# Optimization experiments

Hardware: AMD Instinct MI355X
Metric: run time of the kernel (lower is better)

Reference implementation:

```python
import jax, jax.numpy as jnp
import numpy as np

B = 131072
D_IN = 128
D_H = 128


def _linear_params(key, fan_in, fan_out):
    # mimic nn.Linear init: U(-1/sqrt(fan_in), 1/sqrt(fan_in))
    kw, kb = jax.random.split(key)
    bound = 1.0 / np.sqrt(fan_in)
    W = jax.random.uniform(kw, (fan_in, fan_out), minval=-bound, maxval=bound, dtype=jnp.float32)
    b = jax.random.uniform(kb, (fan_out,), minval=-bound, maxval=bound, dtype=jnp.float32)
    return W, b


def setup_inputs() -> dict:
    key = jax.random.key(0)
    ks = jax.random.split(key, 12)
    inp = {
        'input': jax.random.normal(ks[0], (B, D_IN), dtype=jnp.float32),
        'seq_input': jax.random.normal(ks[1], (B, D_IN), dtype=jnp.float32),
        'hidden': jax.random.normal(ks[2], (B, D_H), dtype=jnp.float32),
    }
    names = ['ir', 'iz', 'in_', 'sr', 'sz', 'sn', 'hr', 'hz', 'hn']
    for i, nm in enumerate(names):
        fan_in = D_H if nm.startswith('h') else D_IN
        W, b = _linear_params(ks[3 + i], fan_in, D_H)
        inp['W_' + nm] = W
        inp['b_' + nm] = b
    return inp


def reference(input, seq_input, hidden,
              W_ir, b_ir, W_iz, b_iz, W_in_, b_in_,
              W_sr, b_sr, W_sz, b_sz, W_sn, b_sn,
              W_hr, b_hr, W_hz, b_hz, W_hn, b_hn):
    def lin(x, W, b):
        return x @ W + b

    hr = lin(hidden, W_hr, b_hr)  # shared between r_input and r_seq
    r_input = jax.nn.sigmoid(lin(input, W_ir, b_ir) + hr)
    r_seq = jax.nn.sigmoid(lin(seq_input, W_sr, b_sr) + hr)
    r = (r_input + r_seq) * 0.5

    hz = lin(hidden, W_hz, b_hz)
    z_input = jax.nn.sigmoid(lin(input, W_iz, b_iz) + hz)
    z_seq = jax.nn.sigmoid(lin(seq_input, W_sz, b_sz) + hz)
    z = (z_input + z_seq) * 0.5

    n = jnp.tanh(lin(input, W_in_, b_in_) + lin(seq_input, W_sn, b_sn)
                 + lin(r * hidden, W_hn, b_hn))
    new_hidden = (1.0 - z) * n + z * hidden
    return new_hidden
```

## Files before the change

kernel.cpp:

```cpp
#include <hip/hip_runtime.h>

#define BDIM 512
#define PACK_BDIM 256

typedef __attribute__((ext_vector_type(8))) short bf16x8;
typedef __attribute__((ext_vector_type(4))) float f32x4;
typedef __attribute__((ext_vector_type(4))) unsigned int u32x4;

__device__ __forceinline__ unsigned short f2b(float x) {
    unsigned u = __float_as_uint(x);
    return (unsigned short)((u + 0x7fffu + ((u >> 16) & 1u)) >> 16);
}
__device__ __forceinline__ float b2f(unsigned short b) {
    return __uint_as_float(((unsigned)b) << 16);
}

typedef __attribute__((address_space(1))) const unsigned int ga_u32;
typedef __attribute__((address_space(3))) unsigned int la_u32;
__device__ __forceinline__ void gload_lds16(const void* g, void* l) {
    __builtin_amdgcn_global_load_lds((ga_u32*)g, (la_u32*)l, 16, 0, 0);
}

__global__ __launch_bounds__(PACK_BDIM) void pack_weights(
    const float* __restrict__ w0, const float* __restrict__ w1,
    const float* __restrict__ w2, const float* __restrict__ w3,
    const float* __restrict__ w4, const float* __restrict__ w5,
    const float* __restrict__ w6, const float* __restrict__ w7,
    const float* __restrict__ w8,
    const float* __restrict__ b0, const float* __restrict__ b1,
    const float* __restrict__ b2, const float* __restrict__ b3,
    const float* __restrict__ b4, const float* __restrict__ b5,
    const float* __restrict__ b6, const float* __restrict__ b7,
    const float* __restrict__ b8, unsigned short* __restrict__ wp)
{
    __shared__ float wsm[16384];
    const float* W; const float* Bp;
    switch (blockIdx.x) {
        case 0: W = w0; Bp = b0; break; case 1: W = w1; Bp = b1; break;
        case 2: W = w2; Bp = b2; break; case 3: W = w3; Bp = b3; break;
        case 4: W = w4; Bp = b4; break; case 5: W = w5; Bp = b5; break;
        case 6: W = w6; Bp = b6; break; case 7: W = w7; Bp = b7; break;
        default: W = w8; Bp = b8; break;
    }
    const int tid = threadIdx.x;
    for (int i = tid; i < 16384; i += PACK_BDIM) wsm[i] = W[i];
    float* biasf = (float*)(wp + 294912);
    if (tid < 128) biasf[blockIdx.x * 128 + tid] = Bp[tid];
    __syncthreads();
    unsigned short* dst = wp + (size_t)blockIdx.x * 32768;
    for (int item = tid; item < 4096; item += PACK_BDIM) {
        const int lane = item & 63, q = item >> 6;
        const int s = q >> 5, cf = q & 31, c = cf >> 3, f = cf & 7;
        const int k0 = c * 32 + (lane >> 4) * 8;
        const int n  = f * 16 + (lane & 15);
        unsigned v2[4];
        for (int i2 = 0; i2 < 4; i2++) {
            unsigned short lohi[2];
            for (int t = 0; t < 2; t++) {
                float x = wsm[(k0 + i2 * 2 + t) * 128 + n];
                unsigned short hb = f2b(x);
                if (s) { hb = (unsigned short)(__float_as_uint(x - b2f(hb)) >> 16); }
                lohi[t] = hb;
            }
            v2[i2] = (unsigned)lohi[0] | ((unsigned)lohi[1] << 16);
        }
        u32x4 vv; vv[0] = v2[0]; vv[1] = v2[1]; vv[2] = v2[2]; vv[3] = v2[3];
        *(u32x4*)(dst + (size_t)(s * 32 + cf) * 512 + lane * 8) = vv;
    }
}

__global__ __launch_bounds__(BDIM) __attribute__((amdgpu_waves_per_eu(4)))
void gru_fused(
    const float* __restrict__ inp, const float* __restrict__ seqp,
    const float* __restrict__ hid, const unsigned short* __restrict__ wp,
    float* __restrict__ outp)
{
    __shared__ __align__(16) unsigned short wbuf[2][16384];
    float* tb = (float*)wbuf[1];

    const int tid    = threadIdx.x;
    const int lane   = tid & 63;
    const int wid    = tid >> 6;
    const int rowgrp = wid >> 1;
    const int colgrp = wid & 1;
    const int agrp   = lane >> 4;
    const int a16    = lane & 15;
    const int ncol0  = colgrp * 64;
    const size_t row0 = (size_t)blockIdx.x * 64;
    const int locrow_a = rowgrp * 16 + a16;
    const int rswA = (locrow_a & 7) << 3;

    const float* pAin  = inp  + (row0 + locrow_a) * 128;
    const float* pAseq = seqp + (row0 + locrow_a) * 128;
    const float* pAhid = hid  + (row0 + locrow_a) * 128;
    const float* biasf = (const float*)(wp + 294912);

    f32x4 hx[4], s1[4], nacc[4], G[4];
    u32x4 ahs[4];
    const f32x4 zv = {0.f, 0.f, 0.f, 0.f};

    auto stageu = [&](int g, int s, int b) {
        const char* src = (const char*)wp + (size_t)g * 65536 + (size_t)s * 32768;
        char* dstb = (char*)wbuf[b];
        #pragma unroll
        for (int j = 0; j < 4; j++) {
            const int off = (j * 8 + wid) * 1024;
            gload_lds16(src + off + lane * 16, dstb + off);
        }
    };

    auto splitc = [&](int c, f32x4 x0, f32x4 x1) -> u32x4 {
        u32x4 a, l;
        #pragma unroll
        for (int p = 0; p < 2; p++) {
            unsigned e0 = __float_as_uint(x0[2 * p]);
            unsigned e1 = __float_as_uint(x0[2 * p + 1]);
            a[p] = __builtin_amdgcn_perm(e1, e0, 0x07060302u);
            float d0 = x0[2 * p]     - __uint_as_float(e0 & 0xffff0000u);
            float d1 = x0[2 * p + 1] - __uint_as_float(e1 & 0xffff0000u);
            l[p] = __builtin_amdgcn_perm(__float_as_uint(d1), __float_as_uint(d0), 0x07060302u);
            unsigned f0 = __float_as_uint(x1[2 * p]);
            unsigned f1 = __float_as_uint(x1[2 * p + 1]);
            a[2 + p] = __builtin_amdgcn_perm(f1, f0, 0x07060302u);
            float g0 = x1[2 * p]     - __uint_as_float(f0 & 0xffff0000u);
            float g1 = x1[2 * p + 1] - __uint_as_float(f1 & 0xffff0000u);
            l[2 + p] = __builtin_amdgcn_perm(__float_as_uint(g1), __float_as_uint(g0), 0x07060302u);
        }
        ahs[c] = a;
        return l;
    };

    auto hiU = [&](const float* pA) {
        #pragma unroll
        for (int f = 0; f < 4; f++) G[f] = zv;
        const unsigned short* wb = wbuf[0];
        #pragma unroll
        for (int c = 0; c < 4; c++) {
            const float* p = pA + c * 32 + agrp * 8;
            u32x4 alp = splitc(c, *(const f32x4*)(p), *(const f32x4*)(p + 4));
            const bf16x8 ah = *(const bf16x8*)&ahs[c];
            const bf16x8 al = *(const bf16x8*)&alp;
            __builtin_amdgcn_s_setprio(1);
            #pragma unroll
            for (int f = 0; f < 4; f++) {
                const int fglob = colgrp * 4 + f;
                const bf16x8 wh = *(const bf16x8*)(&wb[(size_t)(c * 8 + fglob) * 512 + lane * 8]);
                G[f] = __builtin_amdgcn_mfma_f32_16x16x32_bf16(ah, wh, G[f], 0, 0, 0);
                G[f] = __builtin_amdgcn_mfma_f32_16x16x32_bf16(al, wh, G[f], 0, 0, 0);
            }
            __builtin_amdgcn_s_setprio(0);
        }
    };

    auto hiU_lds = [&]() {
        #pragma unroll
        for (int f = 0; f < 4; f++) G[f] = zv;
        const unsigned short* wb = wbuf[0];
        #pragma unroll
        for (int c = 0; c < 4; c++) {
            const int rk = (c * 32 + agrp * 8) ^ rswA;
            f32x4 x0 = *(const f32x4*)(&tb[locrow_a * 128 + rk]);
            f32x4 x1 = *(const f32x4*)(&tb[locrow_a * 128 + rk + 4]);
            u32x4 alp = splitc(c, x0, x1);
            const bf16x8 ah = *(const bf16x8*)&ahs[c];
            const bf16x8 al = *(const bf16x8*)&alp;
            __builtin_amdgcn_s_setprio(1);
            #pragma unroll
            for (int f = 0; f < 4; f++) {
                const int fglob = colgrp * 4 + f;
                const bf16x8 wh = *(const bf16x8*)(&wb[(size_t)(c * 8 + fglob) * 512 + lane * 8]);
                G[f] = __builtin_amdgcn_mfma_f32_16x16x32_bf16(ah, wh, G[f], 0, 0, 0);
                G[f] = __builtin_amdgcn_mfma_f32_16x16x32_bf16(al, wh, G[f], 0, 0, 0);
            }
            __builtin_amdgcn_s_setprio(0);
        }
    };

    auto loU = [&](int g) {
        const unsigned short* wb = wbuf[1];
        __builtin_amdgcn_s_setprio(1);
        #pragma unroll
        for (int c = 0; c < 4; c++) {
            const bf16x8 ah = *(const bf16x8*)&ahs[c];
            #pragma unroll
            for (int f = 0; f < 4; f++) {
                const int fglob = colgrp * 4 + f;
                const bf16x8 wl = *(const bf16x8*)(&wb[(size_t)(c * 8 + fglob) * 512 + lane * 8]);
                G[f] = __builtin_amdgcn_mfma_f32_16x16x32_bf16(ah, wl, G[f], 0, 0, 0);
            }
        }
        __builtin_amdgcn_s_setprio(0);
        #pragma unroll
        for (int f = 0; f < 4; f++) {
            float bv = biasf[g * 128 + ncol0 + f * 16 + a16];
            #pragma unroll
            for (int j = 0; j < 4; j++) G[f][j] += bv;
        }
    };

    auto sigm = [](float x) { return 1.f / (1.f + __expf(-x)); };
    auto tanh_ = [](float x) {
        x = fminf(18.f, fmaxf(-18.f, x));
        float e = __expf(2.f * x);
        return (e - 1.f) / (e + 1.f);
    };

    const unsigned long long GT = 0x417528306ULL;
    stageu(6, 0, 0);

    #pragma clang loop unroll(disable)
    for (int u = 0; u < 9; ++u) {
        const int g = (int)((GT >> (4 * u)) & 15);
        if (u == 3) {
            __syncthreads();
            hiU_lds();
            __syncthreads();
            stageu(g, 1, 1);
        } else {
            __syncthreads();
            stageu(g, 1, 1);
            const float* pA = (u == 0 || u == 6) ? pAhid
                            : (u == 1 || u == 4 || u == 7) ? pAin : pAseq;
            hiU(pA);
        }
        __syncthreads();
        if (u < 8) stageu((int)((GT >> (4 * (u + 1))) & 15), 0, 0);
        loU(g);
        switch (u) {
            case 0: case 6:
                #pragma unroll
                for (int f = 0; f < 4; f++) hx[f] = G[f];
                break;
            case 1: case 7:
                #pragma unroll
                for (int f = 0; f < 4; f++)
                    #pragma unroll
                    for (int j = 0; j < 4; j++)
                        s1[f][j] = sigm(G[f][j] + hx[f][j]);
                break;
            case 2: {
                __syncthreads();
                #pragma unroll
                for (int f = 0; f < 4; f++)
                    #pragma unroll
                    for (int j = 0; j < 4; j++) {
                        int row = rowgrp * 16 + agrp * 4 + j;
                        int col = ncol0 + f * 16 + a16;
                        float r = 0.5f * (s1[f][j] + sigm(G[f][j] + hx[f][j]));
                        float h = hid[(row0 + row) * 128 + col];
                        tb[row * 128 + (col ^ ((row & 7) << 3))] = r * h;
                    }
                break;
            }
            case 3:
                #pragma unroll
                for (int f = 0; f < 4; f++) nacc[f] = G[f];
                break;
            case 4: case 5:
                #pragma unroll
                for (int f = 0; f < 4; f++) nacc[f] += G[f];
                break;
            default:
                break;
        }
    }

    __syncthreads();
    #pragma unroll
    for (int f = 0; f < 4; f++)
        #pragma unroll
        for (int j = 0; j < 4; j++) {
            int row = rowgrp * 16 + agrp * 4 + j;
            int col = ncol0 + f * 16 + a16;
            float zz = 0.5f * (s1[f][j] + sigm(G[f][j] + hx[f][j]));
            float h  = hid[(row0 + row) * 128 + col];
            float nn = tanh_(nacc[f][j]);
            tb[row * 128 + (col ^ ((row & 7) << 3))] = (1.f - zz) * nn + zz * h;
        }
    __syncthreads();
    #pragma unroll
    for (int p = 0; p < 4; p++) {
        int e = p * 2048 + tid * 4;
        int rrow = e >> 7, c0 = e & 127;
        f32x4 v = *(const f32x4*)(&tb[rrow * 128 + (c0 ^ ((rrow & 7) << 3))]);
        *(f32x4*)(&outp[(row0 + rrow) * 128 + c0]) = v;
    }
}

extern "C" void kernel_launch(void* const* d_in, const int* in_sizes, int n_in,
                              void* d_out, int out_size, void* d_ws, size_t ws_size,
                              hipStream_t stream)
{
    (void)in_sizes; (void)n_in; (void)out_size; (void)ws_size;
    const float* inp  = (const float*)d_in[0];
    const float* seqp = (const float*)d_in[1];
    const float* hid  = (const float*)d_in[2];
    const float* W[9]; const float* Bv[9];
    for (int i = 0; i < 9; i++) {
        W[i]  = (const float*)d_in[3 + 2 * i];
        Bv[i] = (const float*)d_in[4 + 2 * i];
    }
    unsigned short* wp = (unsigned short*)d_ws;

    pack_weights<<<9, PACK_BDIM, 0, stream>>>(W[0], W[1], W[2], W[3], W[4],
                                              W[5], W[6], W[7], W[8],
                                              Bv[0], Bv[1], Bv[2], Bv[3], Bv[4],
                                              Bv[5], Bv[6], Bv[7], Bv[8], wp);
    gru_fused<<<2048, BDIM, 0, stream>>>(inp, seqp, hid, wp, (float*)d_out);
}
```

Baseline: 283.3 us.

## Drop low-half weight split; use single bf16 weights with double-buffered staging

```diff
diff --git a/kernel.cpp b/kernel.cpp
--- a/kernel.cpp
+++ b/kernel.cpp
@@ -10,9 +10,6 @@
 __device__ __forceinline__ unsigned short f2b(float x) {
     unsigned u = __float_as_uint(x);
     return (unsigned short)((u + 0x7fffu + ((u >> 16) & 1u)) >> 16);
-}
-__device__ __forceinline__ float b2f(unsigned short b) {
-    return __uint_as_float(((unsigned)b) << 16);
 }
 
 typedef __attribute__((address_space(1))) const unsigned int ga_u32;
@@ -44,28 +41,22 @@
     }
     const int tid = threadIdx.x;
     for (int i = tid; i < 16384; i += PACK_BDIM) wsm[i] = W[i];
-    float* biasf = (float*)(wp + 294912);
+    float* biasf = (float*)(wp + 147456);
     if (tid < 128) biasf[blockIdx.x * 128 + tid] = Bp[tid];
     __syncthreads();
-    unsigned short* dst = wp + (size_t)blockIdx.x * 32768;
-    for (int item = tid; item < 4096; item += PACK_BDIM) {
-        const int lane = item & 63, q = item >> 6;
-        const int s = q >> 5, cf = q & 31, c = cf >> 3, f = cf & 7;
+    unsigned short* dst = wp + (size_t)blockIdx.x * 16384;
+    for (int item = tid; item < 2048; item += PACK_BDIM) {
+        const int lane = item & 63, cf = item >> 6;
+        const int c = cf >> 3, f = cf & 7;
         const int k0 = c * 32 + (lane >> 4) * 8;
         const int n  = f * 16 + (lane & 15);
-        unsigned v2[4];
+        u32x4 vv;
         for (int i2 = 0; i2 < 4; i2++) {
-            unsigned short lohi[2];
-            for (int t = 0; t < 2; t++) {
-                float x = wsm[(k0 + i2 * 2 + t) * 128 + n];
-                unsigned short hb = f2b(x);
-                if (s) { hb = (unsigned short)(__float_as_uint(x - b2f(hb)) >> 16); }
-                lohi[t] = hb;
-            }
-            v2[i2] = (unsigned)lohi[0] | ((unsigned)lohi[1] << 16);
-        }
-        u32x4 vv; vv[0] = v2[0]; vv[1] = v2[1]; vv[2] = v2[2]; vv[3] = v2[3];
-        *(u32x4*)(dst + (size_t)(s * 32 + cf) * 512 + lane * 8) = vv;
+            unsigned short lo = f2b(wsm[(k0 + 2 * i2)     * 128 + n]);
+            unsigned short hi = f2b(wsm[(k0 + 2 * i2 + 1) * 128 + n]);
+            vv[i2] = (unsigned)lo | ((unsigned)hi << 16);
+        }
+        *(u32x4*)(dst + (size_t)cf * 512 + lane * 8) = vv;
     }
 }
 
@@ -76,7 +67,8 @@
     float* __restrict__ outp)
 {
     __shared__ __align__(16) unsigned short wbuf[2][16384];
-    float* tb = (float*)wbuf[1];
+    float* tbR = (float*)wbuf[1];
+    float* tbO = (float*)wbuf[0];
 
     const int tid    = threadIdx.x;
     const int lane   = tid & 63;
@@ -93,14 +85,13 @@
     const float* pAin  = inp  + (row0 + locrow_a) * 128;
     const float* pAseq = seqp + (row0 + locrow_a) * 128;
     const float* pAhid = hid  + (row0 + locrow_a) * 128;
-    const float* biasf = (const float*)(wp + 294912);
+    const float* biasf = (const float*)(wp + 147456);
 
     f32x4 hx[4], s1[4], nacc[4], G[4];
-    u32x4 ahs[4];
     const f32x4 zv = {0.f, 0.f, 0.f, 0.f};
 
-    auto stageu = [&](int g, int s, int b) {
-        const char* src = (const char*)wp + (size_t)g * 65536 + (size_t)s * 32768;
+    auto stageu = [&](int g, int b) {
+        const char* src = (const char*)wp + (size_t)g * 32768;
         char* dstb = (char*)wbuf[b];
         #pragma unroll
         for (int j = 0; j < 4; j++) {
@@ -109,7 +100,7 @@
         }
     };
 
-    auto splitc = [&](int c, f32x4 x0, f32x4 x1) -> u32x4 {
+    auto splitc2 = [&](f32x4 x0, f32x4 x1, bf16x8& ah, bf16x8& al) {
         u32x4 a, l;
         #pragma unroll
         for (int p = 0; p < 2; p++) {
@@ -126,70 +117,58 @@
             float g1 = x1[2 * p + 1] - __uint_as_float(f1 & 0xffff0000u);
             l[2 + p] = __builtin_amdgcn_perm(__float_as_uint(g1), __float_as_uint(g0), 0x07060302u);
         }
-        ahs[c] = a;
-        return l;
-    };
-
-    auto hiU = [&](const float* pA) {
+        ah = *(const bf16x8*)&a;
+        al = *(const bf16x8*)&l;
+    };
+
+    auto gemmG = [&](int b, const float* pA, int g) {
+        #pragma unroll
+        for (int f = 0; f < 4; f++) G[f] = zv;
+        const unsigned short* wb = wbuf[b];
+        #pragma unroll
+        for (int c = 0; c < 4; c++) {
+            const float* p = pA + c * 32 + agrp * 8;
+            bf16x8 ah, al;
+            splitc2(*(const f32x4*)(p), *(const f32x4*)(p + 4), ah, al);
+            __builtin_amdgcn_s_setprio(1);
+            #pragma unroll
+            for (int f = 0; f < 4; f++) {
+                const int fglob = colgrp * 4 + f;
+                const bf16x8 w = *(const bf16x8*)(&wb[(size_t)(c * 8 + fglob) * 512 + lane * 8]);
+                G[f] = __builtin_amdgcn_mfma_f32_16x16x32_bf16(ah, w, G[f], 0, 0, 0);
+                G[f] = __builtin_amdgcn_mfma_f32_16x16x32_bf16(al, w, G[f], 0, 0, 0);
+            }
+            __builtin_amdgcn_s_setprio(0);
+        }
+        #pragma unroll
+        for (int f = 0; f < 4; f++) {
+            float bv = biasf[g * 128 + ncol0 + f * 16 + a16];
+            #pragma unroll
+            for (int j = 0; j < 4; j++) G[f][j] += bv;
+        }
+    };
+
+    auto gemmL = [&](int g) {
         #pragma unroll
         for (int f = 0; f < 4; f++) G[f] = zv;
         const unsigned short* wb = wbuf[0];
         #pragma unroll
         for (int c = 0; c < 4; c++) {
-            const float* p = pA + c * 32 + agrp * 8;
-            u32x4 alp = splitc(c, *(const f32x4*)(p), *(const f32x4*)(p + 4));
-            const bf16x8 ah = *(const bf16x8*)&ahs[c];
-            const bf16x8 al = *(const bf16x8*)&alp;
+            const int rk = (c * 32 + agrp * 8) ^ rswA;
+            f32x4 x0 = *(const f32x4*)(&tbR[locrow_a * 128 + rk]);
+            f32x4 x1 = *(const f32x4*)(&tbR[locrow_a * 128 + rk + 4]);
+            bf16x8 ah, al;
+            splitc2(x0, x1, ah, al);
             __builtin_amdgcn_s_setprio(1);
             #pragma unroll
             for (int f = 0; f < 4; f++) {
                 const int fglob = colgrp * 4 + f;
-                const bf16x8 wh = *(const bf16x8*)(&wb[(size_t)(c * 8 + fglob) * 512 + lane * 8]);
-                G[f] = __builtin_amdgcn_mfma_f32_16x16x32_bf16(ah, wh, G[f], 0, 0, 0);
-                G[f] = __builtin_amdgcn_mfma_f32_16x16x32_bf16(al, wh, G[f], 0, 0, 0);
+                const bf16x8 w = *(const bf16x8*)(&wb[(size_t)(c * 8 + fglob) * 512 + lane * 8]);
+                G[f] = __builtin_amdgcn_mfma_f32_16x16x32_bf16(ah, w, G[f], 0, 0, 0);
+                G[f] = __builtin_amdgcn_mfma_f32_16x16x32_bf16(al, w, G[f], 0, 0, 0);
             }
             __builtin_amdgcn_s_setprio(0);
         }
-    };
-
-    auto hiU_lds = [&]() {
-        #pragma unroll
-        for (int f = 0; f < 4; f++) G[f] = zv;
-        const unsigned short* wb = wbuf[0];
-        #pragma unroll
-        for (int c = 0; c < 4; c++) {
-            const int rk = (c * 32 + agrp * 8) ^ rswA;
-            f32x4 x0 = *(const f32x4*)(&tb[locrow_a * 128 + rk]);
-            f32x4 x1 = *(const f32x4*)(&tb[locrow_a * 128 + rk + 4]);
-            u32x4 alp = splitc(c, x0, x1);
-            const bf16x8 ah = *(const bf16x8*)&ahs[c];
-            const bf16x8 al = *(const bf16x8*)&alp;
-            __builtin_amdgcn_s_setprio(1);
-            #pragma unroll
-            for (int f = 0; f < 4; f++) {
-                const int fglob = colgrp * 4 + f;
-                const bf16x8 wh = *(const bf16x8*)(&wb[(size_t)(c * 8 + fglob) * 512 + lane * 8]);
-                G[f] = __builtin_amdgcn_mfma_f32_16x16x32_bf16(ah, wh, G[f], 0, 0, 0);
-                G[f] = __builtin_amdgcn_mfma_f32_16x16x32_bf16(al, wh, G[f], 0, 0, 0);
-            }
-            __builtin_amdgcn_s_setprio(0);
-        }
-    };
-
-    auto loU = [&](int g) {
-        const unsigned short* wb = wbuf[1];
-        __builtin_amdgcn_s_setprio(1);
-        #pragma unroll
-        for (int c = 0; c < 4; c++) {
-            const bf16x8 ah = *(const bf16x8*)&ahs[c];
-            #pragma unroll
-            for (int f = 0; f < 4; f++) {
-                const int fglob = colgrp * 4 + f;
-                const bf16x8 wl = *(const bf16x8*)(&wb[(size_t)(c * 8 + fglob) * 512 + lane * 8]);
-                G[f] = __builtin_amdgcn_mfma_f32_16x16x32_bf16(ah, wl, G[f], 0, 0, 0);
-            }
-        }
-        __builtin_amdgcn_s_setprio(0);
         #pragma unroll
         for (int f = 0; f < 4; f++) {
             float bv = biasf[g * 128 + ncol0 + f * 16 + a16];
@@ -206,26 +185,22 @@
     };
 
     const unsigned long long GT = 0x417528306ULL;
-    stageu(6, 0, 0);
+    const unsigned CBT = 0x152u;
+    stageu(6, 0);
 
     #pragma clang loop unroll(disable)
     for (int u = 0; u < 9; ++u) {
         const int g = (int)((GT >> (4 * u)) & 15);
+        __syncthreads();
         if (u == 3) {
-            __syncthreads();
-            hiU_lds();
-            __syncthreads();
-            stageu(g, 1, 1);
+            gemmL(g);
         } else {
-            __syncthreads();
-            stageu(g, 1, 1);
+            if (u != 2 && u != 8)
+                stageu((int)((GT >> (4 * (u + 1))) & 15), (CBT >> (u + 1)) & 1);
             const float* pA = (u == 0 || u == 6) ? pAhid
                             : (u == 1 || u == 4 || u == 7) ? pAin : pAseq;
-            hiU(pA);
-        }
-        __syncthreads();
-        if (u < 8) stageu((int)((GT >> (4 * (u + 1))) & 15), 0, 0);
-        loU(g);
+            gemmG((CBT >> u) & 1, pA, g);
+        }
         switch (u) {
             case 0: case 6:
                 #pragma unroll
@@ -239,7 +214,6 @@
                         s1[f][j] = sigm(G[f][j] + hx[f][j]);
                 break;
             case 2: {
-                __syncthreads();
                 #pragma unroll
                 for (int f = 0; f < 4; f++)
                     #pragma unroll
@@ -248,7 +222,7 @@
                         int col = ncol0 + f * 16 + a16;
                         float r = 0.5f * (s1[f][j] + sigm(G[f][j] + hx[f][j]));
                         float h = hid[(row0 + row) * 128 + col];
-                        tb[row * 128 + (col ^ ((row & 7) << 3))] = r * h;
+                        tbR[row * 128 + (col ^ ((row & 7) << 3))] = r * h;
                     }
                 break;
             }
@@ -263,9 +237,10 @@
             default:
                 break;
         }
-    }
-
-    __syncthreads();
+        if (u == 2) { __syncthreads(); stageu(8, 0); }
+        if (u == 3) { __syncthreads(); stageu(2, 1); }
+    }
+
     #pragma unroll
     for (int f = 0; f < 4; f++)
         #pragma unroll
@@ -275,14 +250,14 @@
             float zz = 0.5f * (s1[f][j] + sigm(G[f][j] + hx[f][j]));
             float h  = hid[(row0 + row) * 128 + col];
             float nn = tanh_(nacc[f][j]);
-            tb[row * 128 + (col ^ ((row & 7) << 3))] = (1.f - zz) * nn + zz * h;
+            tbO[row * 128 + (col ^ ((row & 7) << 3))] = (1.f - zz) * nn + zz * h;
         }
     __syncthreads();
     #pragma unroll
     for (int p = 0; p < 4; p++) {
         int e = p * 2048 + tid * 4;
         int rrow = e >> 7, c0 = e & 127;
-        f32x4 v = *(const f32x4*)(&tb[rrow * 128 + (c0 ^ ((rrow & 7) << 3))]);
+        f32x4 v = *(const f32x4*)(&tbO[rrow * 128 + (c0 ^ ((rrow & 7) << 3))]);
         *(f32x4*)(&outp[(row0 + rrow) * 128 + c0]) = v;
     }
 }
```

Measured after the change: 302.4 us. +6.7%, slower.
